# Optimization experiments

Measured on AMD Instinct MI355X. Metric: run time of the kernel, lower is better.

The kernel has to match this reference:

```python
import jax, jax.numpy as jnp
import numpy as np

B, T, D_MODEL, STATE = 4, 4096, 1024, 256
LN_EPS = 1e-5


def setup_inputs() -> dict:
    key = jax.random.key(0)
    ks = jax.random.split(key, 8)
    x = jax.random.normal(ks[0], (B, T, D_MODEL), dtype=jnp.float32)
    bound_d = 1.0 / np.sqrt(D_MODEL)
    bound_n = 1.0 / np.sqrt(STATE)
    Wa_w = jax.random.normal(ks[1], (STATE, D_MODEL), dtype=jnp.float32) * 0.02
    Wa_b = jnp.zeros((STATE,), dtype=jnp.float32)
    WB_w = jax.random.normal(ks[2], (STATE, D_MODEL), dtype=jnp.float32) * 0.02
    WB_b = jax.random.uniform(ks[3], (STATE,), jnp.float32, -bound_d, bound_d)
    WC_w = jax.random.normal(ks[4], (D_MODEL, STATE), dtype=jnp.float32) * 0.02
    WC_b = jax.random.uniform(ks[5], (D_MODEL,), jnp.float32, -bound_n, bound_n)
    log_gamma = jnp.asarray(0.0, dtype=jnp.float32)
    D_skip = jax.random.normal(ks[6], (D_MODEL,), dtype=jnp.float32) * 0.01
    ln_w = jnp.ones((D_MODEL,), dtype=jnp.float32)
    ln_b = jnp.zeros((D_MODEL,), dtype=jnp.float32)
    return {"x": x, "Wa_w": Wa_w, "Wa_b": Wa_b, "log_gamma": log_gamma,
            "WB_w": WB_w, "WB_b": WB_b, "WC_w": WC_w, "WC_b": WC_b,
            "D_skip": D_skip, "ln_w": ln_w, "ln_b": ln_b}


def _layernorm(x, w, b):
    mu = jnp.mean(x, axis=-1, keepdims=True)
    var = jnp.mean(jnp.square(x - mu), axis=-1, keepdims=True)
    return (x - mu) * jax.lax.rsqrt(var + LN_EPS) * w + b


def reference(x, Wa_w, Wa_b, log_gamma, WB_w, WB_b, WC_w, WC_b, D_skip, ln_w, ln_b):
    residual = x
    xn = _layernorm(x, ln_w, ln_b)                      # (B,T,D)
    # Fourier eigenvalues: gamma * tanh(W_a x), FFT, magnitude-contracting scale
    gamma = jax.nn.sigmoid(log_gamma)
    a = gamma * jnp.tanh(jnp.einsum('btd,nd->btn', xn, Wa_w) + Wa_b)  # (B,T,n) real
    a_hat = jnp.fft.fft(a, axis=-1)                     # (B,T,n) complex, conj-symmetric
    mag = jnp.maximum(jnp.abs(a_hat), 1e-8)
    a_hat = a_hat * jax.nn.sigmoid(2.0 * (1.0 - mag))
    # Input projection in Fourier domain
    u = jnp.einsum('btd,nd->btn', xn, WB_w) + WB_b
    u_hat = jnp.fft.fft(u, axis=-1)                     # (B,T,n) complex
    # Linear recurrence h_t = a_t * h_{t-1} + b_t via associative scan over time
    def combine(c1, c2):
        a1, b1 = c1
        a2, b2 = c2
        return (a1 * a2, a2 * b1 + b2)
    _, h_hat = jax.lax.associative_scan(combine, (a_hat, u_hat), axis=1)
    h = jnp.real(jnp.fft.ifft(h_hat, axis=-1)).astype(x.dtype)        # (B,T,n)
    y = jnp.einsum('btn,dn->btd', h, WC_w) + WC_b + D_skip * residual
    return y
```

## Files before the change

### kernel.cpp

```cpp
#include <hip/hip_runtime.h>


typedef unsigned short ushort_t;
typedef short s16x8 __attribute__((ext_vector_type(8)));
typedef float f32x4 __attribute__((ext_vector_type(4)));
typedef _Float16 f16x8 __attribute__((ext_vector_type(8)));
typedef _Float16 f16x2 __attribute__((ext_vector_type(2)));

#define B_ 4
#define T_ 4096
#define D_ 1024
#define N_ 256
#define KB_ 129
#define M_ (B_*T_)

#define SWZ(i) ((i) ^ (((i) >> 3) & 6))
#define DR4(n) ((((n) & 3) << 6) | (((n) & 12) << 2) | (((n) & 48) >> 2) | (((n) >> 6) & 3))

__device__ __forceinline__ ushort_t f2bf(float f) {
  unsigned u = __float_as_uint(f);
  u = (u + 0x7FFFu + ((u >> 16) & 1u)) >> 16;
  return (ushort_t)u;
}
__device__ __forceinline__ float2 cmul(float2 a, float2 b) {
  return make_float2(a.x*b.x - a.y*b.y, a.x*b.y + a.y*b.x);
}
__device__ __forceinline__ float fast_tanh(float x) {
  return 1.f - 2.f / (__expf(2.f * x) + 1.f);
}

typedef const __attribute__((address_space(1))) unsigned glb_u32;
typedef __attribute__((address_space(3))) unsigned lds_u32;
__device__ __forceinline__ void gload16(const void* g, void* l) {
  __builtin_amdgcn_global_load_lds((glb_u32*)g, (lds_u32*)l, 16, 0, 0);
}

__global__ __launch_bounds__(256) void ln_prep_kernel(const float* __restrict__ x,
    const float* __restrict__ w, const float* __restrict__ bb,
    ushort_t* __restrict__ xn,
    const float* __restrict__ Wa, const float* __restrict__ WB,
    const float* __restrict__ WC, ushort_t* __restrict__ Wab,
    ushort_t* __restrict__ WCb) {
  int tid = threadIdx.x;
  if (blockIdx.x >= 4096) {
    int i4 = ((blockIdx.x - 4096) * 256 + tid) * 4;
    float4 v;
    ushort_t* dst;
    if (i4 < 262144)        { v = *(const float4*)(Wa + i4);          dst = Wab + i4; }
    else if (i4 < 524288)   { v = *(const float4*)(WB + i4 - 262144); dst = Wab + i4; }
    else                    { v = *(const float4*)(WC + i4 - 524288); dst = WCb + i4 - 524288; }
    ushort4 o;
    o.x = f2bf(v.x); o.y = f2bf(v.y); o.z = f2bf(v.z); o.w = f2bf(v.w);
    *(ushort4*)dst = o;
    return;
  }
  int lane = tid & 63, wv = tid >> 6;
  int row = blockIdx.x * 4 + wv;
  const float4* xr = (const float4*)(x + (size_t)row * D_);
  float4 v[4];
  float s = 0.f, sq = 0.f;
  #pragma unroll
  for (int j = 0; j < 4; ++j) {
    v[j] = xr[lane + 64 * j];
    s  += v[j].x + v[j].y + v[j].z + v[j].w;
    sq += v[j].x*v[j].x + v[j].y*v[j].y + v[j].z*v[j].z + v[j].w*v[j].w;
  }
  #pragma unroll
  for (int off = 32; off >= 1; off >>= 1) {
    s  += __shfl_xor(s, off);
    sq += __shfl_xor(sq, off);
  }
  float mu  = s * (1.0f / D_);
  float var = sq * (1.0f / D_) - mu * mu;
  float rs  = rsqrtf(var + 1e-5f);
  const float4* w4 = (const float4*)w;
  const float4* b4 = (const float4*)bb;
  ushort4* o4 = (ushort4*)(xn + (size_t)row * D_);
  #pragma unroll
  for (int j = 0; j < 4; ++j) {
    float4 wv_ = w4[lane + 64 * j];
    float4 bv_ = b4[lane + 64 * j];
    ushort4 o;
    o.x = f2bf((v[j].x - mu) * rs * wv_.x + bv_.x);
    o.y = f2bf((v[j].y - mu) * rs * wv_.y + bv_.y);
    o.z = f2bf((v[j].z - mu) * rs * wv_.z + bv_.z);
    o.w = f2bf((v[j].w - mu) * rs * wv_.w + bv_.w);
    o4[lane + 64 * j] = o;
  }
}

template<bool EPI, int BN, bool HOUT>
__global__ __launch_bounds__(256) void gemm_bf16(
    const ushort_t* __restrict__ A, int lda,
    const ushort_t* __restrict__ B, int ldb,
    void* __restrict__ Cv, int ldc,
    int K, int ntiles,
    const float* __restrict__ bias,
    const float* __restrict__ dskip,
    const float* __restrict__ xres) {
  constexpr int NF = BN / 32;
  __shared__ ushort_t Alds[128 * 64];
  __shared__ ushort_t Blds[BN * 64];
  int bid = blockIdx.x;
  int cpx = gridDim.x >> 3;
  bid = (bid & 7) * cpx + (bid >> 3);
  int mt = bid / ntiles, nt = bid % ntiles;
  int m0 = mt * 128, n0 = nt * BN;
  int tid = threadIdx.x;
  int lane = tid & 63, wid = tid >> 6;
  int wm = wid >> 1, wn = wid & 1;

  int lr8 = lane >> 3;
  int gd  = (lane & 7) ^ lr8;
  const ushort_t* gA = A + (size_t)(m0 + wid * 32 + lr8) * lda + gd * 8;
  ushort_t* lA = &Alds[(wid * 32) * 64];
  constexpr int BROWS = BN / 4;
  const ushort_t* gB = B + (size_t)(n0 + wid * BROWS + lr8) * ldb + gd * 8;
  ushort_t* lB = &Blds[(wid * BROWS) * 64];

  f32x4 acc[4][NF] = {};
  int rbase = lane & 15;
  int rb7 = lane & 7;
  int gk0 = lane >> 4;

  for (int k0 = 0; k0 < K; k0 += 64) {
    __syncthreads();
    #pragma unroll
    for (int c = 0; c < 4; ++c)
      gload16(gA + (size_t)(c * 8) * lda + k0, lA + c * 8 * 64);
    #pragma unroll
    for (int c = 0; c < BROWS / 8; ++c)
      gload16(gB + (size_t)(c * 8) * ldb + k0, lB + c * 8 * 64);
    __syncthreads();
    #pragma unroll
    for (int kk = 0; kk < 2; ++kk) {
      int sl = ((gk0 + kk * 4) ^ rb7) * 8;
      s16x8 af[4], bf[NF];
      #pragma unroll
      for (int i = 0; i < 4; ++i)
        af[i] = *reinterpret_cast<const s16x8*>(&Alds[(wm * 64 + i * 16 + rbase) * 64 + sl]);
      #pragma unroll
      for (int j = 0; j < NF; ++j)
        bf[j] = *reinterpret_cast<const s16x8*>(&Blds[(wn * (BN / 2) + j * 16 + rbase) * 64 + sl]);
      #pragma unroll
      for (int i = 0; i < 4; ++i)
        #pragma unroll
        for (int j = 0; j < NF; ++j)
          acc[i][j] = __builtin_amdgcn_mfma_f32_16x16x32_bf16(af[i], bf[j], acc[i][j], 0, 0, 0);
    }
  }

  int r0 = (lane >> 4) * 4, cc = lane & 15;
  #pragma unroll
  for (int i = 0; i < 4; ++i) {
    #pragma unroll
    for (int j = 0; j < NF; ++j) {
      int col = n0 + wn * (BN / 2) + j * 16 + cc;
      #pragma unroll
      for (int r = 0; r < 4; ++r) {
        int row = m0 + wm * 64 + i * 16 + r0 + r;
        float v = acc[i][j][r];
        if constexpr (EPI) v += bias[col] + dskip[col] * xres[(size_t)row * ldc + col];
        if constexpr (HOUT) ((_Float16*)Cv)[(size_t)row * ldc + col] = (_Float16)v;
        else                ((float*)Cv)[(size_t)row * ldc + col] = v;
      }
    }
  }
}

__global__ __launch_bounds__(512) void fft_fwd(const _Float16* __restrict__ au,
    const float* __restrict__ ba, const float* __restrict__ bu,
    const float* __restrict__ lg, _Float16* __restrict__ ah, _Float16* __restrict__ uh) {
  __shared__ float2 Z[8][256];
  __shared__ float2 Tw[256];
  int tid = threadIdx.x;
  int m0 = blockIdx.x * 8;
  int tg = tid >> 6, lane = tid & 63;
  if (tid < 256) {
    float sn, cs;
    __sincosf(-6.2831853071795864f / 256.f * (float)tid, &sn, &cs);
    Tw[tid] = make_float2(cs, sn);
  }
  float gamma = 1.f / (1.f + __expf(-lg[0]));
  const _Float16* row = au + (size_t)(m0 + tg) * (2 * N_);
  #pragma unroll
  for (int j = 0; j < 4; ++j) {
    int n = lane + 64 * j;
    float a = gamma * fast_tanh((float)row[n] + ba[n]);
    float u = (float)row[N_ + n] + bu[n];
    Z[tg][SWZ(DR4(n))] = make_float2(a, u);
  }
  __syncthreads();
  #pragma unroll
  for (int ls = 0; ls < 4; ++ls) {
    const int Q = 1 << (2 * ls);
    const int step = 64 >> (2 * ls);
    int j = lane & (Q - 1);
    int g = lane >> (2 * ls);
    int base = g * (4 * Q) + j;
    float2 a0 = Z[tg][SWZ(base)];
    float2 a1 = Z[tg][SWZ(base + Q)];
    float2 a2 = Z[tg][SWZ(base + 2 * Q)];
    float2 a3 = Z[tg][SWZ(base + 3 * Q)];
    if (ls > 0) {
      int e = j * step;
      a1 = cmul(a1, Tw[e]);
      a2 = cmul(a2, Tw[2 * e]);
      a3 = cmul(a3, Tw[3 * e]);
    }
    float2 t0 = make_float2(a0.x + a2.x, a0.y + a2.y);
    float2 t1 = make_float2(a0.x - a2.x, a0.y - a2.y);
    float2 t2 = make_float2(a1.x + a3.x, a1.y + a3.y);
    float2 d  = make_float2(a1.x - a3.x, a1.y - a3.y);
    float2 t3 = make_float2(d.y, -d.x);
    Z[tg][SWZ(base)]         = make_float2(t0.x + t2.x, t0.y + t2.y);
    Z[tg][SWZ(base + Q)]     = make_float2(t1.x + t3.x, t1.y + t3.y);
    Z[tg][SWZ(base + 2 * Q)] = make_float2(t0.x - t2.x, t0.y - t2.y);
    Z[tg][SWZ(base + 3 * Q)] = make_float2(t1.x - t3.x, t1.y - t3.y);
  }
  __syncthreads();
  int b = m0 >> 12, tb = m0 & (T_ - 1);
  #pragma unroll
  for (int p = 0; p < 3; ++p) {
    int k = (tid >> 3) + p * 64;
    int tl = tid & 7;
    if (k <= 128) {
      float2 zk = Z[tl][SWZ(k)];
      float2 zn = Z[tl][SWZ((256 - k) & 255)];
      float2 Af = make_float2(0.5f * (zk.x + zn.x), 0.5f * (zk.y - zn.y));
      float2 Uf = make_float2(0.5f * (zk.y + zn.y), -0.5f * (zk.x - zn.x));
      float mag = fmaxf(sqrtf(Af.x * Af.x + Af.y * Af.y), 1e-8f);
      float scl = 1.f / (1.f + __expf(-2.f * (1.f - mag)));
      Af.x *= scl; Af.y *= scl;
      size_t off2 = (((size_t)(b * KB_ + k)) * T_ + tb + tl) * 2;
      f16x2 av; av[0] = (_Float16)Af.x; av[1] = (_Float16)Af.y;
      f16x2 uv; uv[0] = (_Float16)Uf.x; uv[1] = (_Float16)Uf.y;
      *(f16x2*)(ah + off2) = av;
      *(f16x2*)(uh + off2) = uv;
    }
  }
}

__global__ __launch_bounds__(512) void scan_kernel(const _Float16* __restrict__ ah,
                                                   _Float16* __restrict__ uh) {
  __shared__ float4 wagg[8];
  int tid = threadIdx.x;
  int lane = tid & 63, wv = tid >> 6;
  size_t base = (size_t)blockIdx.x * T_ * 2;
  const f16x8* a8 = (const f16x8*)(ah + base);
  f16x8* u8 = (f16x8*)(uh + base);
  f16x8 Av[2], Uv[2];
  #pragma unroll
  for (int q = 0; q < 2; ++q) { Av[q] = a8[tid * 2 + q]; Uv[q] = u8[tid * 2 + q]; }
  float2 La[8], Lb[8];
  float2 ra = make_float2(1.f, 0.f), rb = make_float2(0.f, 0.f);
  #pragma unroll
  for (int e = 0; e < 8; ++e) {
    const int q = e >> 2, i = (e & 3) * 2;
    float2 a = make_float2((float)Av[q][i], (float)Av[q][i + 1]);
    float2 u = make_float2((float)Uv[q][i], (float)Uv[q][i + 1]);
    float2 t = cmul(a, rb);
    rb = make_float2(t.x + u.x, t.y + u.y);
    ra = cmul(ra, a);
    La[e] = ra; Lb[e] = rb;
  }
  #pragma unroll
  for (int off = 1; off < 64; off <<= 1) {
    float ax = __shfl_up(ra.x, off, 64), ay = __shfl_up(ra.y, off, 64);
    float bx = __shfl_up(rb.x, off, 64), by = __shfl_up(rb.y, off, 64);
    if (lane >= off) {
      float2 Ap = make_float2(ax, ay), Bp = make_float2(bx, by);
      float2 nB = cmul(ra, Bp);
      nB.x += rb.x; nB.y += rb.y;
      ra = cmul(Ap, ra);
      rb = nB;
    }
  }
  if (lane == 63) wagg[wv] = make_float4(ra.x, ra.y, rb.x, rb.y);
  __syncthreads();
  float2 Bw = make_float2(0.f, 0.f);
  for (int w0 = 0; w0 < wv; ++w0) {
    float4 g = wagg[w0];
    float2 gA = make_float2(g.x, g.y), gB = make_float2(g.z, g.w);
    Bw = cmul(gA, Bw);
    Bw.x += gB.x; Bw.y += gB.y;
  }
  float ax = __shfl_up(ra.x, 1, 64), ay = __shfl_up(ra.y, 1, 64);
  float bx = __shfl_up(rb.x, 1, 64), by = __shfl_up(rb.y, 1, 64);
  float2 Ae, Be;
  if (lane == 0) { Ae = make_float2(1.f, 0.f); Be = make_float2(0.f, 0.f); }
  else           { Ae = make_float2(ax, ay);   Be = make_float2(bx, by);   }
  float2 Pb = cmul(Ae, Bw);
  Pb.x += Be.x; Pb.y += Be.y;
  #pragma unroll
  for (int q = 0; q < 2; ++q) {
    f16x8 o;
    #pragma unroll
    for (int e2 = 0; e2 < 4; ++e2) {
      const int e = q * 4 + e2;
      float2 h = cmul(La[e], Pb);
      h.x += Lb[e].x; h.y += Lb[e].y;
      o[e2 * 2]     = (_Float16)h.x;
      o[e2 * 2 + 1] = (_Float16)h.y;
    }
    u8[tid * 2 + q] = o;
  }
}

__global__ __launch_bounds__(256) void ifft_kernel(const _Float16* __restrict__ hh,
                                                   ushort_t* __restrict__ hb) {
  __shared__ float2 Hraw[8][132];
  __shared__ float2 Wz[4][256];
  __shared__ float2 Tw[256];
  int tid = threadIdx.x;
  int m0 = blockIdx.x * 8;
  int b = m0 >> 12, tb = m0 & (T_ - 1);
  {
    float sn, cs;
    __sincosf(6.2831853071795864f / 256.f * (float)tid, &sn, &cs);
    Tw[tid] = make_float2(cs, sn);
  }
  #pragma unroll
  for (int p = 0; p < 5; ++p) {
    int k = p * 32 + (tid >> 3), tl = tid & 7;
    if (k <= 128) {
      f16x2 hv = *(const f16x2*)(hh + (((size_t)(b * KB_ + k)) * T_ + tb + tl) * 2);
      Hraw[tl][k] = make_float2((float)hv[0], (float)hv[1]);
    }
  }
  __syncthreads();
  #pragma unroll
  for (int p = 0; p < 3; ++p) {
    int idx = p * 256 + tid;
    if (idx < 516) {
      int k = idx >> 2, pr = idx & 3;
      float2 h1 = Hraw[2 * pr][k], h2 = Hraw[2 * pr + 1][k];
      Wz[pr][SWZ(DR4(k))] = make_float2(h1.x - h2.y, h1.y + h2.x);
      if (k >= 1 && k <= 127)
        Wz[pr][SWZ(DR4(256 - k))] = make_float2(h1.x + h2.y, h2.x - h1.y);
    }
  }
  __syncthreads();
  int pr = tid >> 6, lane = tid & 63;
  #pragma unroll
  for (int ls = 0; ls < 4; ++ls) {
    const int Q = 1 << (2 * ls);
    const int step = 64 >> (2 * ls);
    int j = lane & (Q - 1);
    int g = lane >> (2 * ls);
    int base = g * (4 * Q) + j;
    float2 a0 = Wz[pr][SWZ(base)];
    float2 a1 = Wz[pr][SWZ(base + Q)];
    float2 a2 = Wz[pr][SWZ(base + 2 * Q)];
    float2 a3 = Wz[pr][SWZ(base + 3 * Q)];
    if (ls > 0) {
      int e = j * step;
      a1 = cmul(a1, Tw[e]);
      a2 = cmul(a2, Tw[2 * e]);
      a3 = cmul(a3, Tw[3 * e]);
    }
    float2 t0 = make_float2(a0.x + a2.x, a0.y + a2.y);
    float2 t1 = make_float2(a0.x - a2.x, a0.y - a2.y);
    float2 t2 = make_float2(a1.x + a3.x, a1.y + a3.y);
    float2 d  = make_float2(a1.x - a3.x, a1.y - a3.y);
    float2 t3 = make_float2(-d.y, d.x);
    Wz[pr][SWZ(base)]         = make_float2(t0.x + t2.x, t0.y + t2.y);
    Wz[pr][SWZ(base + Q)]     = make_float2(t1.x + t3.x, t1.y + t3.y);
    Wz[pr][SWZ(base + 2 * Q)] = make_float2(t0.x - t2.x, t0.y - t2.y);
    Wz[pr][SWZ(base + 3 * Q)] = make_float2(t1.x - t3.x, t1.y - t3.y);
  }
  const float inv = 1.f / 256.f;
  #pragma unroll
  for (int j = 0; j < 4; ++j) {
    int n = lane + 64 * j;
    float2 wv = Wz[pr][SWZ(n)];
    hb[(size_t)(m0 + 2 * pr) * N_ + n]     = f2bf(wv.x * inv);
    hb[(size_t)(m0 + 2 * pr + 1) * N_ + n] = f2bf(wv.y * inv);
  }
}

extern "C" void kernel_launch(void* const* d_in, const int* in_sizes, int n_in,
                              void* d_out, int out_size, void* d_ws, size_t ws_size,
                              hipStream_t stream) {
  const float* x      = (const float*)d_in[0];
  const float* Wa_w   = (const float*)d_in[1];
  const float* Wa_b   = (const float*)d_in[2];
  const float* lg     = (const float*)d_in[3];
  const float* WB_w   = (const float*)d_in[4];
  const float* WB_b   = (const float*)d_in[5];
  const float* WC_w   = (const float*)d_in[6];
  const float* WC_b   = (const float*)d_in[7];
  const float* D_skip = (const float*)d_in[8];
  const float* ln_w   = (const float*)d_in[9];
  const float* ln_b   = (const float*)d_in[10];
  float* out = (float*)d_out;
  char* ws = (char*)d_ws;

  ushort_t*  xn  = (ushort_t*)(ws + 0);
  ushort_t*  Wab = (ushort_t*)(ws + 33554432);
  ushort_t*  WCb = (ushort_t*)(ws + 34603008);
  _Float16*  au  = (_Float16*)(ws + 35127296);
  ushort_t*  hb  = (ushort_t*)(ws + 35127296);
  _Float16*  ah  = (_Float16*)(ws + 0);
  _Float16*  uh  = (_Float16*)(ws + 16908288);

  ln_prep_kernel<<<4864, 256, 0, stream>>>(x, ln_w, ln_b, xn,
                                           Wa_w, WB_w, WC_w, Wab, WCb);
  gemm_bf16<false, 64, true><<<1024, 256, 0, stream>>>(xn, D_, Wab, D_, au, 512,
                                                       D_, 8, nullptr, nullptr, nullptr);
  fft_fwd<<<M_ / 8, 512, 0, stream>>>(au, Wa_b, WB_b, lg, ah, uh);
  scan_kernel<<<B_ * KB_, 512, 0, stream>>>(ah, uh);
  ifft_kernel<<<M_ / 8, 256, 0, stream>>>(uh, hb);
  gemm_bf16<true, 128, false><<<1024, 256, 0, stream>>>(hb, N_, WCb, N_, out, D_,
                                                        N_, 8, WC_b, D_skip, x);
}
```

Baseline: 108.1 us.

## Fuse LayerNorm apply into first GEMM A-tile load, keep only per-row stats

The prep kernel now computes only per-row mean and rsqrt and no longer writes a normalized bf16 copy of x. The first GEMM reads fp32 x directly, normalizes and converts it to bf16 into LDS, and loads only the weight tile asynchronously. This removes the 32MB xn write and its 32MB re-read. In exchange the GEMM reads fp32 x (double the bytes of bf16) through synchronous register loads, losing the async global-to-LDS path for A. The second GEMM is specialized with constants and hoists the bias, skip and residual loads in its epilogue.

```diff
diff --git a/kernel.cpp b/kernel.cpp
--- a/kernel.cpp
+++ b/kernel.cpp
@@ -35,9 +35,8 @@
   __builtin_amdgcn_global_load_lds((glb_u32*)g, (lds_u32*)l, 16, 0, 0);
 }
 
-__global__ __launch_bounds__(256) void ln_prep_kernel(const float* __restrict__ x,
-    const float* __restrict__ w, const float* __restrict__ bb,
-    ushort_t* __restrict__ xn,
+__global__ __launch_bounds__(256) void stats_prep_kernel(const float* __restrict__ x,
+    float2* __restrict__ stats,
     const float* __restrict__ Wa, const float* __restrict__ WB,
     const float* __restrict__ WC, ushort_t* __restrict__ Wab,
     ushort_t* __restrict__ WCb) {
@@ -57,54 +56,121 @@
   int lane = tid & 63, wv = tid >> 6;
   int row = blockIdx.x * 4 + wv;
   const float4* xr = (const float4*)(x + (size_t)row * D_);
-  float4 v[4];
   float s = 0.f, sq = 0.f;
   #pragma unroll
   for (int j = 0; j < 4; ++j) {
-    v[j] = xr[lane + 64 * j];
-    s  += v[j].x + v[j].y + v[j].z + v[j].w;
-    sq += v[j].x*v[j].x + v[j].y*v[j].y + v[j].z*v[j].z + v[j].w*v[j].w;
+    float4 v = xr[lane + 64 * j];
+    s  += v.x + v.y + v.z + v.w;
+    sq += v.x*v.x + v.y*v.y + v.z*v.z + v.w*v.w;
   }
   #pragma unroll
   for (int off = 32; off >= 1; off >>= 1) {
     s  += __shfl_xor(s, off);
     sq += __shfl_xor(sq, off);
   }
-  float mu  = s * (1.0f / D_);
-  float var = sq * (1.0f / D_) - mu * mu;
-  float rs  = rsqrtf(var + 1e-5f);
-  const float4* w4 = (const float4*)w;
-  const float4* b4 = (const float4*)bb;
-  ushort4* o4 = (ushort4*)(xn + (size_t)row * D_);
-  #pragma unroll
-  for (int j = 0; j < 4; ++j) {
-    float4 wv_ = w4[lane + 64 * j];
-    float4 bv_ = b4[lane + 64 * j];
-    ushort4 o;
-    o.x = f2bf((v[j].x - mu) * rs * wv_.x + bv_.x);
-    o.y = f2bf((v[j].y - mu) * rs * wv_.y + bv_.y);
-    o.z = f2bf((v[j].z - mu) * rs * wv_.z + bv_.z);
-    o.w = f2bf((v[j].w - mu) * rs * wv_.w + bv_.w);
-    o4[lane + 64 * j] = o;
-  }
-}
-
-template<bool EPI, int BN, bool HOUT>
-__global__ __launch_bounds__(256) void gemm_bf16(
-    const ushort_t* __restrict__ A, int lda,
-    const ushort_t* __restrict__ B, int ldb,
-    void* __restrict__ Cv, int ldc,
-    int K, int ntiles,
-    const float* __restrict__ bias,
-    const float* __restrict__ dskip,
+  if (lane == 0) {
+    float mu  = s * (1.0f / D_);
+    float var = sq * (1.0f / D_) - mu * mu;
+    stats[row] = make_float2(mu, rsqrtf(var + 1e-5f));
+  }
+}
+
+__global__ __launch_bounds__(256) void gemm1_ln(
+    const float* __restrict__ x, const float2* __restrict__ stats,
+    const float* __restrict__ lnw, const float* __restrict__ lnb,
+    const ushort_t* __restrict__ B, _Float16* __restrict__ C) {
+  constexpr int NF = 2;
+  __shared__ ushort_t Alds[128 * 64];
+  __shared__ ushort_t Blds[64 * 64];
+  int bid = blockIdx.x;
+  int cpx = gridDim.x >> 3;
+  bid = (bid & 7) * cpx + (bid >> 3);
+  int mt = bid >> 3, nt = bid & 7;
+  int m0 = mt * 128, n0 = nt * 64;
+  int tid = threadIdx.x;
+  int lane = tid & 63, wid = tid >> 6;
+  int wm = wid >> 1, wn = wid & 1;
+
+  int lr8 = lane >> 3;
+  int gd  = (lane & 7) ^ lr8;
+  const ushort_t* gB = B + (size_t)(n0 + wid * 16 + lr8) * D_ + gd * 8;
+  ushort_t* lB = &Blds[(wid * 16) * 64];
+
+  int rsub = tid >> 4, l16 = tid & 15;
+  int slotA = ((l16 >> 1) ^ (rsub & 7)) * 8 + (l16 & 1) * 4;
+  float2 st[8];
+  #pragma unroll
+  for (int it = 0; it < 8; ++it) st[it] = stats[m0 + rsub + it * 16];
+
+  f32x4 acc[4][NF] = {};
+  int rbase = lane & 15;
+  int rb7 = lane & 7;
+  int gk0 = lane >> 4;
+
+  for (int k0 = 0; k0 < D_; k0 += 64) {
+    __syncthreads();
+    float4 wv = *(const float4*)(lnw + k0 + l16 * 4);
+    float4 bv = *(const float4*)(lnb + k0 + l16 * 4);
+    #pragma unroll
+    for (int it = 0; it < 8; ++it) {
+      int r = rsub + it * 16;
+      float4 xv = *(const float4*)(x + (size_t)(m0 + r) * D_ + k0 + l16 * 4);
+      float mu = st[it].x, rs = st[it].y;
+      ushort4 o;
+      o.x = f2bf((xv.x - mu) * rs * wv.x + bv.x);
+      o.y = f2bf((xv.y - mu) * rs * wv.y + bv.y);
+      o.z = f2bf((xv.z - mu) * rs * wv.z + bv.z);
+      o.w = f2bf((xv.w - mu) * rs * wv.w + bv.w);
+      *(ushort4*)(&Alds[r * 64 + slotA]) = o;
+    }
+    #pragma unroll
+    for (int c = 0; c < 2; ++c)
+      gload16(gB + (size_t)(c * 8) * D_ + k0, lB + c * 8 * 64);
+    __syncthreads();
+    #pragma unroll
+    for (int kk = 0; kk < 2; ++kk) {
+      int sl = ((gk0 + kk * 4) ^ rb7) * 8;
+      s16x8 af[4], bf[NF];
+      #pragma unroll
+      for (int i = 0; i < 4; ++i)
+        af[i] = *reinterpret_cast<const s16x8*>(&Alds[(wm * 64 + i * 16 + rbase) * 64 + sl]);
+      #pragma unroll
+      for (int j = 0; j < NF; ++j)
+        bf[j] = *reinterpret_cast<const s16x8*>(&Blds[(wn * 32 + j * 16 + rbase) * 64 + sl]);
+      #pragma unroll
+      for (int i = 0; i < 4; ++i)
+        #pragma unroll
+        for (int j = 0; j < NF; ++j)
+          acc[i][j] = __builtin_amdgcn_mfma_f32_16x16x32_bf16(af[i], bf[j], acc[i][j], 0, 0, 0);
+    }
+  }
+
+  int r0 = (lane >> 4) * 4, cc = lane & 15;
+  #pragma unroll
+  for (int i = 0; i < 4; ++i)
+    #pragma unroll
+    for (int j = 0; j < NF; ++j) {
+      int col = n0 + wn * 32 + j * 16 + cc;
+      #pragma unroll
+      for (int r = 0; r < 4; ++r) {
+        int row = m0 + wm * 64 + i * 16 + r0 + r;
+        C[(size_t)row * 512 + col] = (_Float16)acc[i][j][r];
+      }
+    }
+}
+
+__global__ __launch_bounds__(256) void gemm2_epi(
+    const ushort_t* __restrict__ A, const ushort_t* __restrict__ B,
+    float* __restrict__ C,
+    const float* __restrict__ bias, const float* __restrict__ dskip,
     const float* __restrict__ xres) {
-  constexpr int NF = BN / 32;
+  constexpr int BN = 128, NF = 4;
   __shared__ ushort_t Alds[128 * 64];
   __shared__ ushort_t Blds[BN * 64];
   int bid = blockIdx.x;
   int cpx = gridDim.x >> 3;
   bid = (bid & 7) * cpx + (bid >> 3);
-  int mt = bid / ntiles, nt = bid % ntiles;
+  int mt = bid >> 3, nt = bid & 7;
   int m0 = mt * 128, n0 = nt * BN;
   int tid = threadIdx.x;
   int lane = tid & 63, wid = tid >> 6;
@@ -112,25 +178,23 @@
 
   int lr8 = lane >> 3;
   int gd  = (lane & 7) ^ lr8;
-  const ushort_t* gA = A + (size_t)(m0 + wid * 32 + lr8) * lda + gd * 8;
+  const ushort_t* gA = A + (size_t)(m0 + wid * 32 + lr8) * N_ + gd * 8;
   ushort_t* lA = &Alds[(wid * 32) * 64];
-  constexpr int BROWS = BN / 4;
-  const ushort_t* gB = B + (size_t)(n0 + wid * BROWS + lr8) * ldb + gd * 8;
-  ushort_t* lB = &Blds[(wid * BROWS) * 64];
+  const ushort_t* gB = B + (size_t)(n0 + wid * 32 + lr8) * N_ + gd * 8;
+  ushort_t* lB = &Blds[(wid * 32) * 64];
 
   f32x4 acc[4][NF] = {};
   int rbase = lane & 15;
   int rb7 = lane & 7;
   int gk0 = lane >> 4;
 
-  for (int k0 = 0; k0 < K; k0 += 64) {
+  for (int k0 = 0; k0 < N_; k0 += 64) {
     __syncthreads();
     #pragma unroll
-    for (int c = 0; c < 4; ++c)
-      gload16(gA + (size_t)(c * 8) * lda + k0, lA + c * 8 * 64);
-    #pragma unroll
-    for (int c = 0; c < BROWS / 8; ++c)
-      gload16(gB + (size_t)(c * 8) * ldb + k0, lB + c * 8 * 64);
+    for (int c = 0; c < 4; ++c) {
+      gload16(gA + (size_t)(c * 8) * N_ + k0, lA + c * 8 * 64);
+      gload16(gB + (size_t)(c * 8) * N_ + k0, lB + c * 8 * 64);
+    }
     __syncthreads();
     #pragma unroll
     for (int kk = 0; kk < 2; ++kk) {
@@ -141,7 +205,7 @@
         af[i] = *reinterpret_cast<const s16x8*>(&Alds[(wm * 64 + i * 16 + rbase) * 64 + sl]);
       #pragma unroll
       for (int j = 0; j < NF; ++j)
-        bf[j] = *reinterpret_cast<const s16x8*>(&Blds[(wn * (BN / 2) + j * 16 + rbase) * 64 + sl]);
+        bf[j] = *reinterpret_cast<const s16x8*>(&Blds[(wn * 64 + j * 16 + rbase) * 64 + sl]);
       #pragma unroll
       for (int i = 0; i < 4; ++i)
         #pragma unroll
@@ -151,18 +215,29 @@
   }
 
   int r0 = (lane >> 4) * 4, cc = lane & 15;
+  float bcol[NF], dcol[NF];
+  #pragma unroll
+  for (int j = 0; j < NF; ++j) {
+    int col = n0 + wn * 64 + j * 16 + cc;
+    bcol[j] = bias[col];
+    dcol[j] = dskip[col];
+  }
   #pragma unroll
   for (int i = 0; i < 4; ++i) {
+    float xr[NF][4];
+    #pragma unroll
+    for (int j = 0; j < NF; ++j)
+      #pragma unroll
+      for (int r = 0; r < 4; ++r)
+        xr[j][r] = xres[(size_t)(m0 + wm * 64 + i * 16 + r0 + r) * D_ +
+                        n0 + wn * 64 + j * 16 + cc];
     #pragma unroll
     for (int j = 0; j < NF; ++j) {
-      int col = n0 + wn * (BN / 2) + j * 16 + cc;
+      int col = n0 + wn * 64 + j * 16 + cc;
       #pragma unroll
       for (int r = 0; r < 4; ++r) {
         int row = m0 + wm * 64 + i * 16 + r0 + r;
-        float v = acc[i][j][r];
-        if constexpr (EPI) v += bias[col] + dskip[col] * xres[(size_t)row * ldc + col];
-        if constexpr (HOUT) ((_Float16*)Cv)[(size_t)row * ldc + col] = (_Float16)v;
-        else                ((float*)Cv)[(size_t)row * ldc + col] = v;
+        C[(size_t)row * D_ + col] = acc[i][j][r] + bcol[j] + dcol[j] * xr[j][r];
       }
     }
   }
@@ -396,7 +471,7 @@
   float* out = (float*)d_out;
   char* ws = (char*)d_ws;
 
-  ushort_t*  xn  = (ushort_t*)(ws + 0);
+  float2*    stats = (float2*)(ws + 0);
   ushort_t*  Wab = (ushort_t*)(ws + 33554432);
   ushort_t*  WCb = (ushort_t*)(ws + 34603008);
   _Float16*  au  = (_Float16*)(ws + 35127296);
@@ -404,13 +479,10 @@
   _Float16*  ah  = (_Float16*)(ws + 0);
   _Float16*  uh  = (_Float16*)(ws + 16908288);
 
-  ln_prep_kernel<<<4864, 256, 0, stream>>>(x, ln_w, ln_b, xn,
-                                           Wa_w, WB_w, WC_w, Wab, WCb);
-  gemm_bf16<false, 64, true><<<1024, 256, 0, stream>>>(xn, D_, Wab, D_, au, 512,
-                                                       D_, 8, nullptr, nullptr, nullptr);
+  stats_prep_kernel<<<4864, 256, 0, stream>>>(x, stats, Wa_w, WB_w, WC_w, Wab, WCb);
+  gemm1_ln<<<1024, 256, 0, stream>>>(x, stats, ln_w, ln_b, Wab, au);
   fft_fwd<<<M_ / 8, 512, 0, stream>>>(au, Wa_b, WB_b, lg, ah, uh);
   scan_kernel<<<B_ * KB_, 512, 0, stream>>>(ah, uh);
   ifft_kernel<<<M_ / 8, 256, 0, stream>>>(uh, hb);
-  gemm_bf16<true, 128, false><<<1024, 256, 0, stream>>>(hb, N_, WCb, N_, out, D_,
-                                                        N_, 8, WC_b, D_skip, x);
-}
+  gemm2_epi<<<1024, 256, 0, stream>>>(hb, WCb, out, WC_b, D_skip, x);
+}
```

Result: slower. 130.2 us (+20.5%).
